# Optimization experiments

Measured on AMD Instinct MI355X. Metric: run time of the kernel, lower is better.

Reference implementation:

```python
import jax, jax.numpy as jnp
import numpy as np

N_E = 8192
E_DIM = 256
BETA = 0.25


def setup_inputs() -> dict:
    key = jax.random.key(0)
    kz, ke = jax.random.split(key)
    z = jax.random.normal(kz, (16, E_DIM, 32, 32), dtype=jnp.float32)
    embedding = jax.random.uniform(ke, (N_E, E_DIM), dtype=jnp.float32,
                                   minval=-1.0 / N_E, maxval=1.0 / N_E)
    return {"z": z, "embedding": embedding}


def reference(z, embedding):
    n_e, e_dim = embedding.shape
    # (B, C, H, W) -> (B, H, W, C) -> (N, e_dim)
    zp = jnp.transpose(z, (0, 2, 3, 1))
    zf = zp.reshape(-1, e_dim)
    # squared L2 distances: |z|^2 + |e|^2 - 2 z.e   -> (N, n_e)
    dists = (jnp.sum(zf * zf, axis=1, keepdims=True)
             + jnp.sum(embedding * embedding, axis=1)
             - 2.0 * (zf @ embedding.T))
    # two smallest distances (top-2 of negated dists)
    _, top2_idx = jax.lax.top_k(-dists, 2)
    min_encoding_indices = top2_idx[:, 0:1]
    second_encoding_indices = top2_idx[:, 1:2]
    min_encodings = jax.nn.one_hot(top2_idx[:, 0], n_e, dtype=zp.dtype)  # (N, n_e)
    z_q = (min_encodings @ embedding).reshape(zp.shape)
    # commitment / codebook loss
    loss = (jnp.mean((jax.lax.stop_gradient(z_q) - zp) ** 2)
            + BETA * jnp.mean((z_q - jax.lax.stop_gradient(zp)) ** 2))
    # straight-through estimator
    z_q = zp + jax.lax.stop_gradient(z_q - zp)
    avg_probs = jnp.mean(min_encodings, axis=0)
    perplexity = jnp.exp(-jnp.sum(avg_probs * jnp.log(avg_probs + 1e-10)))
    z_q = jnp.transpose(z_q, (0, 3, 1, 2))
    return (loss, z_q, perplexity, min_encodings,
            min_encoding_indices, second_encoding_indices)
```

## Files before the change

kernel.cpp:

```cpp
#include <hip/hip_runtime.h>
#include <cfloat>
#include <cstdint>
#include <cstddef>

#define M_ROWS 16384
#define NE     8192
#define KD     256

#define OFF_LOSS   0ULL
#define OFF_ZQ     1ULL
#define OFF_PERP   4194305ULL
#define OFF_ONEHOT 4194306ULL
#define OFF_I0     138412034ULL
#define OFF_I1     138428418ULL

#define SCR_Z16  0ULL
#define SCR_E16  2097152ULL
#define SCR_Z32T 3145728ULL
#define SCR_PART 7340032ULL

#define WS_I0    0
#define WS_HIST  16384
#define WS_ENORM 24576
#define WS_CNORM 32768
#define WS_T0SUM 49152
#define WS_TOTAL 49154

typedef _Float16 fp16x8 __attribute__((ext_vector_type(8)));
typedef float    floatx16 __attribute__((ext_vector_type(16)));

__global__ void zero_ws_kernel(float* __restrict__ ws) {
    int i = blockIdx.x * 256 + threadIdx.x;
    if (i < WS_TOTAL) ws[i] = 0.0f;
}

__global__ void zero_onehot_kernel(float* __restrict__ out) {
    size_t tidg = (size_t)blockIdx.x * 1024 + threadIdx.x;
    float4* base = (float4*)(out + OFF_ONEHOT + 2);
    const float4 zz = make_float4(0.f, 0.f, 0.f, 0.f);
#pragma unroll
    for (int i = 0; i < 8; i++) {
        size_t q = tidg + (size_t)i * 4194304ULL;
        if (q < 33554431ULL) base[q] = zz;
    }
    if (tidg == 0) {
        out[OFF_ONEHOT + 0] = 0.f;
        out[OFF_ONEHOT + 1] = 0.f;
        out[OFF_ONEHOT + 134217726ULL] = 0.f;
        out[OFF_ONEHOT + 134217727ULL] = 0.f;
    }
}

__global__ void scatter_ones_kernel(const int* __restrict__ ws_i0, float* __restrict__ out) {
    int r = blockIdx.x * 256 + threadIdx.x;
    int j = ws_i0[r] & (NE - 1);
    out[OFF_ONEHOT + (size_t)r * NE + j] = 1.0f;
}

__device__ __forceinline__ float pairwise16(const float* sq, int lane16) {
    const int h = lane16 >> 3;
    const int j = lane16 & 7;
    float r = sq[h * 128 + j];
#pragma unroll
    for (int i = 1; i < 16; i++) r = r + sq[h * 128 + i * 8 + j];
    float s = r + __shfl_xor(r, 1);
    s = s + __shfl_xor(s, 2);
    s = s + __shfl_xor(s, 4);
    s = s + __shfl_xor(s, 8);
    return s;
}

__global__ void enorm_kernel(const float* __restrict__ emb, float* __restrict__ enorm) {
    __shared__ float sq[16][257];
    const int tid = threadIdx.x;
    const int row0 = blockIdx.x * 16;
#pragma unroll
    for (int p = 0; p < 4; p++) {
        int q = p * 256 + tid;
        int rl = q >> 6, kq = q & 63;
        float4 v = *(const float4*)(emb + (size_t)(row0 + rl) * KD + kq * 4);
        sq[rl][kq * 4 + 0] = v.x * v.x;
        sq[rl][kq * 4 + 1] = v.y * v.y;
        sq[rl][kq * 4 + 2] = v.z * v.z;
        sq[rl][kq * 4 + 3] = v.w * v.w;
    }
    __syncthreads();
    const int rl = tid >> 4, lane16 = tid & 15;
    float s = pairwise16(&sq[rl][0], lane16);
    if (lane16 == 0) enorm[row0 + rl] = s;
}

__global__ void cnorm_kernel(const float* __restrict__ z, float* __restrict__ cnorm) {
    __shared__ float sq[16][257];
    const int tid = threadIdx.x;
    const int r0  = blockIdx.x * 16;
    const int b   = r0 >> 10;
    const int hw0 = r0 & 1023;
    const float* zb = z + ((size_t)b << 18) + hw0;
#pragma unroll
    for (int p = 0; p < 4; p++) {
        int q = p * 256 + tid;
        int c = q >> 2, hq = q & 3;
        float4 v = *(const float4*)(zb + ((size_t)c << 10) + hq * 4);
        sq[hq * 4 + 0][c] = v.x * v.x;
        sq[hq * 4 + 1][c] = v.y * v.y;
        sq[hq * 4 + 2][c] = v.z * v.z;
        sq[hq * 4 + 3][c] = v.w * v.w;
    }
    __syncthreads();
    const int rl = tid >> 4, lane16 = tid & 15;
    float s = pairwise16(&sq[rl][0], lane16);
    if (lane16 == 0) cnorm[r0 + rl] = s;
}

__global__ void split_z_kernel(const float* __restrict__ z, _Float16* __restrict__ z16,
                               float* __restrict__ z32t) {
    __shared__ float tile[64][65];
    const int tid = threadIdx.x;
    const int r0  = blockIdx.x * 64;
    const int kbig = blockIdx.y;
    const int b   = r0 >> 10;
    const int hw0 = r0 & 1023;
#pragma unroll
    for (int p = 0; p < 4; p++) {
        int q = p * 256 + tid;
        int cl = q >> 4, hq = q & 15;
        float4 v = *(const float4*)(z + ((size_t)b << 18) + (size_t)(kbig * 64 + cl) * 1024 + hw0 + hq * 4);
        tile[hq * 4 + 0][cl] = v.x;
        tile[hq * 4 + 1][cl] = v.y;
        tile[hq * 4 + 2][cl] = v.z;
        tile[hq * 4 + 3][cl] = v.w;
    }
    __syncthreads();
#pragma unroll
    for (int p = 0; p < 2; p++) {
        int u = p * 256 + tid;
        int row = u >> 3, k8l = u & 7;
        int r = r0 + row;
        fp16x8 vh;
#pragma unroll
        for (int e = 0; e < 8; e++) vh[e] = (_Float16)tile[row][k8l * 8 + e];
        int kb = kbig * 2 + (k8l >> 2);
        int k8 = k8l & 3;
        size_t unit = ((size_t)(r >> 7) * 8 + kb) * 512 + (size_t)(r & 127) * 4 + (k8 ^ (r & 3));
        *(fp16x8*)(z16 + unit * 8) = vh;
    }
#pragma unroll
    for (int p = 0; p < 4; p++) {
        int q = p * 256 + tid;
        int row = q >> 4, co = (q & 15) * 4;
        float4 v = make_float4(tile[row][co], tile[row][co + 1], tile[row][co + 2], tile[row][co + 3]);
        *(float4*)(z32t + (size_t)(r0 + row) * 256 + kbig * 64 + co) = v;
    }
}

__global__ void split_e_kernel(const float* __restrict__ emb, _Float16* __restrict__ e16) {
    int u = blockIdx.x * 256 + threadIdx.x;
    size_t go = (size_t)u * 8;
    float4 v0 = *(const float4*)(emb + go);
    float4 v1 = *(const float4*)(emb + go + 4);
    float x[8] = {v0.x, v0.y, v0.z, v0.w, v1.x, v1.y, v1.z, v1.w};
    fp16x8 vh;
#pragma unroll
    for (int e = 0; e < 8; e++) vh[e] = (_Float16)(x[e] * 256.0f);
    int code = u >> 5, k8g = u & 31;
    int kb = k8g >> 2, k8 = k8g & 3;
    size_t unit = ((size_t)(code >> 7) * 8 + kb) * 512 + (size_t)(code & 127) * 4 + (k8 ^ (code & 3));
    *(fp16x8*)(e16 + unit * 8) = vh;
}

__device__ __forceinline__ fp16x8 frag_ld(const _Float16* lds, int rc, int ku) {
    int slot = rc * 4 + (ku ^ (rc & 3));
    return *(const fp16x8*)(lds + slot * 8);
}

#define MFMA(d, a, b) d = __builtin_amdgcn_mfma_f32_32x32x16_f16(a, b, d, 0, 0, 0)

__device__ __forceinline__ void ins2(float t, int i, float& t0, int& i0, float& t1, int& i1) {
    if (t < t0 || (t == t0 && i < i0)) { t1 = t0; i1 = i0; t0 = t; i0 = i; }
    else if (t < t1 || (t == t1 && i < i1)) { t1 = t; i1 = i; }
}

__launch_bounds__(256, 3)
__global__ void mfma_top2_kernel(const _Float16* __restrict__ e16, const _Float16* __restrict__ z16,
                                 const float* __restrict__ enorm_g, const float* __restrict__ cnorm_g,
                                 float4* __restrict__ part) {
    __shared__ _Float16 As[2][4096];
    __shared__ _Float16 Bs[2][4096];
    __shared__ float enb[128];
    __shared__ float mbuf[128][4];

    const int tid = threadIdx.x;
    const int lane = tid & 63, wid = tid >> 6;
    const int l31 = lane & 31, half = lane >> 5;
    const int wave_m = wid & 1, wave_n = wid >> 1;
    const int mtile = blockIdx.x;
    const int ntile = blockIdx.y;

    const float4* Ap = (const float4*)(e16 + (size_t)mtile * 8 * 512 * 8);
    const float4* Bp = (const float4*)(z16 + (size_t)ntile * 8 * 512 * 8);

    if (tid < 128) enb[tid] = enorm_g[mtile * 128 + tid];
    float Cn[2];
    Cn[0] = cnorm_g[ntile * 128 + wave_n * 64 + l31];
    Cn[1] = cnorm_g[ntile * 128 + wave_n * 64 + 32 + l31];

    const int rcA0 = wave_m * 64 + l31, rcA1 = rcA0 + 32;
    const int rcB0 = wave_n * 64 + l31, rcB1 = rcB0 + 32;

    {
        float4 ra0 = Ap[tid], ra1 = Ap[256 + tid];
        float4 rb0 = Bp[tid], rb1 = Bp[256 + tid];
        ((float4*)As[0])[tid] = ra0; ((float4*)As[0])[256 + tid] = ra1;
        ((float4*)Bs[0])[tid] = rb0; ((float4*)Bs[0])[256 + tid] = rb1;
    }
    __syncthreads();

    floatx16 acc00 = (floatx16)0.f, acc01 = (floatx16)0.f,
             acc10 = (floatx16)0.f, acc11 = (floatx16)0.f;

    for (int kb = 0; kb < 8; kb++) {
        const int cur = kb & 1;
        float4 ra0, ra1, rb0, rb1;
        if (kb < 7) {
            const int nb = (kb + 1) * 512;
            ra0 = Ap[nb + tid]; ra1 = Ap[nb + 256 + tid];
            rb0 = Bp[nb + tid]; rb1 = Bp[nb + 256 + tid];
        }
#pragma unroll
        for (int ks = 0; ks < 2; ks++) {
            const int ku = ks * 2 + half;
            fp16x8 a0 = frag_ld(As[cur], rcA0, ku);
            fp16x8 a1 = frag_ld(As[cur], rcA1, ku);
            fp16x8 b0 = frag_ld(Bs[cur], rcB0, ku);
            fp16x8 b1 = frag_ld(Bs[cur], rcB1, ku);
            MFMA(acc00, a0, b0);
            MFMA(acc01, a0, b1);
            MFMA(acc10, a1, b0);
            MFMA(acc11, a1, b1);
        }
        if (kb < 7) {
            ((float4*)As[cur ^ 1])[tid] = ra0; ((float4*)As[cur ^ 1])[256 + tid] = ra1;
            ((float4*)Bs[cur ^ 1])[tid] = rb0; ((float4*)Bs[cur ^ 1])[256 + tid] = rb1;
        }
        __syncthreads();
    }

    float t0s[2] = {FLT_MAX, FLT_MAX}, t1s[2] = {FLT_MAX, FLT_MAX};
    int   i0s[2] = {0x7fffffff, 0x7fffffff}, i1s[2] = {0x7fffffff, 0x7fffffff};
#pragma unroll
    for (int mt = 0; mt < 2; mt++) {
#pragma unroll
        for (int reg = 0; reg < 16; reg++) {
            const int rl = (reg & 3) + 8 * (reg >> 2) + 4 * half;
            const int cloc = wave_m * 64 + mt * 32 + rl;
            const int code = mtile * 128 + cloc;
            const float E = enb[cloc];
            float g0 = (mt == 0) ? acc00[reg] : acc10[reg];
            float g1 = (mt == 0) ? acc01[reg] : acc11[reg];
            ins2(fmaf(-0.0078125f, g0, Cn[0] + E), code, t0s[0], i0s[0], t1s[0], i1s[0]);
            ins2(fmaf(-0.0078125f, g1, Cn[1] + E), code, t0s[1], i0s[1], t1s[1], i1s[1]);
        }
    }
#pragma unroll
    for (int s = 0; s < 2; s++) {
        float o0 = __shfl_xor(t0s[s], 32), o1 = __shfl_xor(t1s[s], 32);
        int  oi0 = __shfl_xor(i0s[s], 32), oi1 = __shfl_xor(i1s[s], 32);
        ins2(o0, oi0, t0s[s], i0s[s], t1s[s], i1s[s]);
        ins2(o1, oi1, t0s[s], i0s[s], t1s[s], i1s[s]);
    }
    __syncthreads();
    if (wave_m == 1 && lane < 32) {
#pragma unroll
        for (int s = 0; s < 2; s++) {
            int zr = wave_n * 64 + s * 32 + l31;
            mbuf[zr][0] = t0s[s]; mbuf[zr][1] = t1s[s];
            mbuf[zr][2] = __int_as_float(i0s[s]); mbuf[zr][3] = __int_as_float(i1s[s]);
        }
    }
    __syncthreads();
    if (wave_m == 0 && lane < 32) {
#pragma unroll
        for (int s = 0; s < 2; s++) {
            int zr = wave_n * 64 + s * 32 + l31;
            ins2(mbuf[zr][0], __float_as_int(mbuf[zr][2]), t0s[s], i0s[s], t1s[s], i1s[s]);
            ins2(mbuf[zr][1], __float_as_int(mbuf[zr][3]), t0s[s], i0s[s], t1s[s], i1s[s]);
            float4 o;
            o.x = t0s[s]; o.y = t1s[s];
            o.z = __int_as_float(i0s[s]); o.w = __int_as_float(i1s[s]);
            part[(size_t)(ntile * 128 + zr) * 64 + mtile] = o;
        }
    }
}

__global__ void rescore_kernel(const float* __restrict__ z32t, const float* __restrict__ emb,
                               const float* __restrict__ enorm_g, const float* __restrict__ cnorm_g,
                               const float4* __restrict__ part, float* __restrict__ out,
                               int* __restrict__ ws_i0, int* __restrict__ hist,
                               double* __restrict__ t0sum) {
    const int tid  = threadIdx.x;
    const int lane = tid & 63, wid = tid >> 6;
    const int r = blockIdx.x * 4 + wid;

    const int c4 = lane * 4;
    float4 zv = *(const float4*)(z32t + (size_t)r * 256 + c4);
    const double zv0 = (double)zv.x, zv1 = (double)zv.y, zv2 = (double)zv.z, zv3 = (double)zv.w;

    float m1 = FLT_MAX, m2 = FLT_MAX;
    for (int g = 0; g < 64; g++) {
        float4 p = part[(size_t)r * 64 + g];
        if (p.x < m1) { m2 = m1; m1 = p.x; } else if (p.x < m2) m2 = p.x;
        if (p.y < m1) { m2 = m1; m1 = p.y; } else if (p.y < m2) m2 = p.y;
    }
    const float T = m2 + 1.2e-4f;
    const float C = cnorm_g[r];

    float bt0 = FLT_MAX, bt1 = FLT_MAX;
    int   bi0 = NE - 1, bi1 = NE - 1;
    for (int g = 0; g < 64; g++) {
        float4 p = part[(size_t)r * 64 + g];
        float tv[2] = {p.x, p.y};
        int   jv[2] = {__float_as_int(p.z), __float_as_int(p.w)};
#pragma unroll
        for (int e = 0; e < 2; e++) {
            if (tv[e] <= T) {
                const int j = jv[e] & (NE - 1);
                float4 ev = *(const float4*)(emb + ((size_t)j << 8) + c4);
                double gl = zv0 * (double)ev.x + zv1 * (double)ev.y +
                            zv2 * (double)ev.z + zv3 * (double)ev.w;
#pragma unroll
                for (int m = 1; m < 64; m <<= 1) gl += __shfl_xor(gl, m);
                float g2 = (float)(2.0 * gl);
                float S = C + enorm_g[j];
                float tex = S - g2;
                if (tex < bt0 || (tex == bt0 && j < bi0)) {
                    bt1 = bt0; bi1 = bi0; bt0 = tex; bi0 = j;
                } else if (tex < bt1 || (tex == bt1 && j < bi1)) {
                    bt1 = tex; bi1 = j;
                }
            }
        }
    }

    if (lane == 0) {
        out[OFF_I0 + r] = (float)bi0;
        out[OFF_I1 + r] = (float)bi1;
        ws_i0[r] = bi0;
        atomicAdd(&hist[bi0], 1);
    }
    __shared__ double red[4];
    if (lane == 0) red[wid] = (double)bt0;
    __syncthreads();
    if (tid == 0) atomicAdd(t0sum, (red[0] + red[1]) + (red[2] + red[3]));
}

__global__ void zq_kernel(const float* __restrict__ emb, const int* __restrict__ ws_i0,
                          float* __restrict__ out) {
    __shared__ float zt[64][65];
    const int tid = threadIdx.x;
    const int r0  = blockIdx.x * 64;
    const int b   = r0 >> 10;
    const int hw0 = r0 & 1023;
    const int kb  = blockIdx.y;
#pragma unroll
    for (int p = 0; p < 4; p++) {
        int q = p * 256 + tid;
        int row = q >> 4, co = (q & 15) * 4;
        int idx = ws_i0[r0 + row] & (NE - 1);
        float4 v = *(const float4*)(emb + ((size_t)idx << 8) + kb * 64 + co);
        zt[row][co + 0] = v.x; zt[row][co + 1] = v.y;
        zt[row][co + 2] = v.z; zt[row][co + 3] = v.w;
    }
    __syncthreads();
#pragma unroll
    for (int p = 0; p < 4; p++) {
        int q = p * 256 + tid;
        int c = q >> 4, h4 = (q & 15) * 4;
        float4 v = make_float4(zt[h4 + 0][c], zt[h4 + 1][c], zt[h4 + 2][c], zt[h4 + 3][c]);
        *(float4*)(out + OFF_ZQ + (((size_t)b * 256 + kb * 64 + c) << 10) + hw0 + h4) = v;
    }
}

__global__ void finalize_kernel(const int* __restrict__ hist, const double* __restrict__ t0sum,
                                float* __restrict__ out) {
    __shared__ float red[256];
    float s = 0.f;
    for (int j = threadIdx.x; j < NE; j += 256) {
        float p = (float)hist[j] * (1.0f / 16384.0f);
        s += p * logf(p + 1e-10f);
    }
    red[threadIdx.x] = s;
    __syncthreads();
    for (int m = 128; m; m >>= 1) {
        if (threadIdx.x < m) red[threadIdx.x] += red[threadIdx.x + m];
        __syncthreads();
    }
    if (threadIdx.x == 0) {
        out[OFF_PERP] = expf(-red[0]);
        out[OFF_LOSS] = 1.25f * (float)(t0sum[0] * (1.0 / 4194304.0));
    }
}

extern "C" void kernel_launch(void* const* d_in, const int* in_sizes, int n_in,
                              void* d_out, int out_size, void* d_ws, size_t ws_size,
                              hipStream_t stream) {
    const float* z   = (const float*)d_in[0];
    const float* emb = (const float*)d_in[1];
    float* out = (float*)d_out;
    float* ws  = (float*)d_ws;

    int*    ws_i0    = (int*)ws + WS_I0;
    int*    ws_hist  = (int*)ws + WS_HIST;
    float*  ws_enorm = ws + WS_ENORM;
    float*  ws_cnorm = ws + WS_CNORM;
    double* ws_t0sum = (double*)(ws + WS_T0SUM);

    float* scr = out + OFF_ONEHOT + 2;
    _Float16* z16 = (_Float16*)(scr + SCR_Z16);
    _Float16* e16 = (_Float16*)(scr + SCR_E16);
    float*  z32t  = scr + SCR_Z32T;
    float4* part  = (float4*)(scr + SCR_PART);

    hipLaunchKernelGGL(zero_ws_kernel, dim3(194), dim3(256), 0, stream, ws);
    hipLaunchKernelGGL(enorm_kernel, dim3(512), dim3(256), 0, stream, emb, ws_enorm);
    hipLaunchKernelGGL(cnorm_kernel, dim3(1024), dim3(256), 0, stream, z, ws_cnorm);
    hipLaunchKernelGGL(split_z_kernel, dim3(256, 4), dim3(256), 0, stream, z, z16, z32t);
    hipLaunchKernelGGL(split_e_kernel, dim3(1024), dim3(256), 0, stream, emb, e16);
    hipLaunchKernelGGL(mfma_top2_kernel, dim3(64, 128), dim3(256), 0, stream,
                       e16, z16, ws_enorm, ws_cnorm, part);
    hipLaunchKernelGGL(rescore_kernel, dim3(4096), dim3(256), 0, stream,
                       z32t, emb, ws_enorm, ws_cnorm, part, out, ws_i0, ws_hist, ws_t0sum);
    hipLaunchKernelGGL(zero_onehot_kernel, dim3(4096), dim3(1024), 0, stream, out);
    hipLaunchKernelGGL(scatter_ones_kernel, dim3(64), dim3(256), 0, stream, ws_i0, out);
    hipLaunchKernelGGL(zq_kernel, dim3(256, 4), dim3(256), 0, stream, emb, ws_i0, out);
    hipLaunchKernelGGL(finalize_kernel, dim3(1), dim3(256), 0, stream,
                       ws_hist, ws_t0sum, out);
}
```

Baseline: 1.160 ms.

## Fuse norm and split kernels, remap GEMM blocks per XCD, parallelize rescore scan

Folds the embedding and z norm kernels and the workspace zeroing into the fp16 split kernels, so each input is read once and fewer kernels are launched. The MFMA top-2 kernel moves to a 1-D grid whose blocks are remapped so that each XCD works on a contiguous group of z tiles, aiming at better L2 reuse, and its occupancy hint is raised from 3 to 4 blocks. The rescore kernel now loads the 64 partial results in parallel across lanes, finds the threshold with a wave-wide shuffle reduction, and visits candidates through ballot masks instead of two serial 64-step loops. The higher occupancy target may force register spills, and the fused split_z kernel uses a large shared-memory tile of about 67 KB per block.

Measured after the change: 1.074 ms. 7.4% less time.

```diff
diff --git a/kernel.cpp b/kernel.cpp
--- a/kernel.cpp
+++ b/kernel.cpp
@@ -29,11 +29,6 @@
 typedef _Float16 fp16x8 __attribute__((ext_vector_type(8)));
 typedef float    floatx16 __attribute__((ext_vector_type(16)));
 
-__global__ void zero_ws_kernel(float* __restrict__ ws) {
-    int i = blockIdx.x * 256 + threadIdx.x;
-    if (i < WS_TOTAL) ws[i] = 0.0f;
-}
-
 __global__ void zero_onehot_kernel(float* __restrict__ out) {
     size_t tidg = (size_t)blockIdx.x * 1024 + threadIdx.x;
     float4* base = (float4*)(out + OFF_ONEHOT + 2);
@@ -57,21 +52,27 @@
     out[OFF_ONEHOT + (size_t)r * NE + j] = 1.0f;
 }
 
-__device__ __forceinline__ float pairwise16(const float* sq, int lane16) {
-    const int h = lane16 >> 3;
-    const int j = lane16 & 7;
-    float r = sq[h * 128 + j];
-#pragma unroll
-    for (int i = 1; i < 16; i++) r = r + sq[h * 128 + i * 8 + j];
-    float s = r + __shfl_xor(r, 1);
-    s = s + __shfl_xor(s, 2);
-    s = s + __shfl_xor(s, 4);
-    s = s + __shfl_xor(s, 8);
+__device__ __forceinline__ float pairwise16_sq(const float* row, int lane16) {
+    const int h = lane16 >> 3, j = lane16 & 7;
+    const float* p = row + h * 128 + j;
+    float x = p[0];
+    float r = __fmul_rn(x, x);
+#pragma unroll
+    for (int i = 1; i < 16; i++) {
+        float y = p[i * 8];
+        r = __fadd_rn(r, __fmul_rn(y, y));
+    }
+    float s = __fadd_rn(r, __shfl_xor(r, 1));
+    s = __fadd_rn(s, __shfl_xor(s, 2));
+    s = __fadd_rn(s, __shfl_xor(s, 4));
+    s = __fadd_rn(s, __shfl_xor(s, 8));
     return s;
 }
 
-__global__ void enorm_kernel(const float* __restrict__ emb, float* __restrict__ enorm) {
-    __shared__ float sq[16][257];
+__global__ void split_e_kernel(const float* __restrict__ emb, _Float16* __restrict__ e16,
+                               float* __restrict__ enorm, int* __restrict__ hist,
+                               float* __restrict__ wsf) {
+    __shared__ float ef[16][261];
     const int tid = threadIdx.x;
     const int row0 = blockIdx.x * 16;
 #pragma unroll
@@ -79,94 +80,73 @@
         int q = p * 256 + tid;
         int rl = q >> 6, kq = q & 63;
         float4 v = *(const float4*)(emb + (size_t)(row0 + rl) * KD + kq * 4);
-        sq[rl][kq * 4 + 0] = v.x * v.x;
-        sq[rl][kq * 4 + 1] = v.y * v.y;
-        sq[rl][kq * 4 + 2] = v.z * v.z;
-        sq[rl][kq * 4 + 3] = v.w * v.w;
-    }
-    __syncthreads();
-    const int rl = tid >> 4, lane16 = tid & 15;
-    float s = pairwise16(&sq[rl][0], lane16);
-    if (lane16 == 0) enorm[row0 + rl] = s;
-}
-
-__global__ void cnorm_kernel(const float* __restrict__ z, float* __restrict__ cnorm) {
-    __shared__ float sq[16][257];
+        ef[rl][kq * 4 + 0] = v.x; ef[rl][kq * 4 + 1] = v.y;
+        ef[rl][kq * 4 + 2] = v.z; ef[rl][kq * 4 + 3] = v.w;
+    }
+    __syncthreads();
+#pragma unroll
+    for (int p = 0; p < 2; p++) {
+        int u = p * 256 + tid;
+        int rl = u >> 5, k8g = u & 31;
+        int code = row0 + rl;
+        fp16x8 vh;
+#pragma unroll
+        for (int e = 0; e < 8; e++) vh[e] = (_Float16)(ef[rl][k8g * 8 + e] * 256.0f);
+        int kb = k8g >> 2, k8 = k8g & 3;
+        size_t unit = ((size_t)(code >> 7) * 8 + kb) * 512 + (size_t)(code & 127) * 4 + (k8 ^ (code & 3));
+        *(fp16x8*)(e16 + unit * 8) = vh;
+    }
+    {
+        int rl = tid >> 4, lane16 = tid & 15;
+        float s = pairwise16_sq(&ef[rl][0], lane16);
+        if (lane16 == 0) enorm[row0 + rl] = s;
+    }
+    if (blockIdx.x < 32) hist[blockIdx.x * 256 + tid] = 0;
+    if (blockIdx.x == 32 && tid < 2) wsf[WS_T0SUM + tid] = 0.0f;
+}
+
+__global__ void split_z_kernel(const float* __restrict__ z, _Float16* __restrict__ z16,
+                               float* __restrict__ z32t, float* __restrict__ cnorm) {
+    __shared__ float zf[64][261];
     const int tid = threadIdx.x;
-    const int r0  = blockIdx.x * 16;
+    const int r0  = blockIdx.x * 64;
     const int b   = r0 >> 10;
     const int hw0 = r0 & 1023;
     const float* zb = z + ((size_t)b << 18) + hw0;
 #pragma unroll
-    for (int p = 0; p < 4; p++) {
+    for (int p = 0; p < 16; p++) {
         int q = p * 256 + tid;
-        int c = q >> 2, hq = q & 3;
+        int c = q >> 4, hq = q & 15;
         float4 v = *(const float4*)(zb + ((size_t)c << 10) + hq * 4);
-        sq[hq * 4 + 0][c] = v.x * v.x;
-        sq[hq * 4 + 1][c] = v.y * v.y;
-        sq[hq * 4 + 2][c] = v.z * v.z;
-        sq[hq * 4 + 3][c] = v.w * v.w;
-    }
-    __syncthreads();
-    const int rl = tid >> 4, lane16 = tid & 15;
-    float s = pairwise16(&sq[rl][0], lane16);
-    if (lane16 == 0) cnorm[r0 + rl] = s;
-}
-
-__global__ void split_z_kernel(const float* __restrict__ z, _Float16* __restrict__ z16,
-                               float* __restrict__ z32t) {
-    __shared__ float tile[64][65];
-    const int tid = threadIdx.x;
-    const int r0  = blockIdx.x * 64;
-    const int kbig = blockIdx.y;
-    const int b   = r0 >> 10;
-    const int hw0 = r0 & 1023;
-#pragma unroll
-    for (int p = 0; p < 4; p++) {
-        int q = p * 256 + tid;
-        int cl = q >> 4, hq = q & 15;
-        float4 v = *(const float4*)(z + ((size_t)b << 18) + (size_t)(kbig * 64 + cl) * 1024 + hw0 + hq * 4);
-        tile[hq * 4 + 0][cl] = v.x;
-        tile[hq * 4 + 1][cl] = v.y;
-        tile[hq * 4 + 2][cl] = v.z;
-        tile[hq * 4 + 3][cl] = v.w;
-    }
-    __syncthreads();
-#pragma unroll
-    for (int p = 0; p < 2; p++) {
+        zf[hq * 4 + 0][c] = v.x; zf[hq * 4 + 1][c] = v.y;
+        zf[hq * 4 + 2][c] = v.z; zf[hq * 4 + 3][c] = v.w;
+    }
+    __syncthreads();
+#pragma unroll
+    for (int rr = 0; rr < 4; rr++) {
+        int row = rr * 16 + (tid >> 4);
+        float s = pairwise16_sq(&zf[row][0], tid & 15);
+        if ((tid & 15) == 0) cnorm[r0 + row] = s;
+    }
+#pragma unroll
+    for (int p = 0; p < 8; p++) {
         int u = p * 256 + tid;
-        int row = u >> 3, k8l = u & 7;
+        int row = u >> 5, k8g = u & 31;
         int r = r0 + row;
         fp16x8 vh;
 #pragma unroll
-        for (int e = 0; e < 8; e++) vh[e] = (_Float16)tile[row][k8l * 8 + e];
-        int kb = kbig * 2 + (k8l >> 2);
-        int k8 = k8l & 3;
+        for (int e = 0; e < 8; e++) vh[e] = (_Float16)zf[row][k8g * 8 + e];
+        int kb = k8g >> 2, k8 = k8g & 3;
         size_t unit = ((size_t)(r >> 7) * 8 + kb) * 512 + (size_t)(r & 127) * 4 + (k8 ^ (r & 3));
         *(fp16x8*)(z16 + unit * 8) = vh;
     }
 #pragma unroll
-    for (int p = 0; p < 4; p++) {
+    for (int p = 0; p < 16; p++) {
         int q = p * 256 + tid;
-        int row = q >> 4, co = (q & 15) * 4;
-        float4 v = make_float4(tile[row][co], tile[row][co + 1], tile[row][co + 2], tile[row][co + 3]);
-        *(float4*)(z32t + (size_t)(r0 + row) * 256 + kbig * 64 + co) = v;
-    }
-}
-
-__global__ void split_e_kernel(const float* __restrict__ emb, _Float16* __restrict__ e16) {
-    int u = blockIdx.x * 256 + threadIdx.x;
-    size_t go = (size_t)u * 8;
-    float4 v0 = *(const float4*)(emb + go);
-    float4 v1 = *(const float4*)(emb + go + 4);
-    float x[8] = {v0.x, v0.y, v0.z, v0.w, v1.x, v1.y, v1.z, v1.w};
-    fp16x8 vh;
-#pragma unroll
-    for (int e = 0; e < 8; e++) vh[e] = (_Float16)(x[e] * 256.0f);
-    int code = u >> 5, k8g = u & 31;
-    int kb = k8g >> 2, k8 = k8g & 3;
-    size_t unit = ((size_t)(code >> 7) * 8 + kb) * 512 + (size_t)(code & 127) * 4 + (k8 ^ (code & 3));
-    *(fp16x8*)(e16 + unit * 8) = vh;
+        int row = q >> 6, co = (q & 63) * 4;
+        float4 v = make_float4(zf[row][co], zf[row][co + 1], zf[row][co + 2], zf[row][co + 3]);
+        *(float4*)(z32t + (size_t)(r0 + row) * 256 + co) = v;
+    }
 }
 
 __device__ __forceinline__ fp16x8 frag_ld(const _Float16* lds, int rc, int ku) {
@@ -181,7 +161,7 @@
     else if (t < t1 || (t == t1 && i < i1)) { t1 = t; i1 = i; }
 }
 
-__launch_bounds__(256, 3)
+__launch_bounds__(256, 4)
 __global__ void mfma_top2_kernel(const _Float16* __restrict__ e16, const _Float16* __restrict__ z16,
                                  const float* __restrict__ enorm_g, const float* __restrict__ cnorm_g,
                                  float4* __restrict__ part) {
@@ -194,8 +174,10 @@
     const int lane = tid & 63, wid = tid >> 6;
     const int l31 = lane & 31, half = lane >> 5;
     const int wave_m = wid & 1, wave_n = wid >> 1;
-    const int mtile = blockIdx.x;
-    const int ntile = blockIdx.y;
+    const int id = blockIdx.x;
+    const int xcd = id & 7, slot = id >> 3;
+    const int mtile = slot >> 4;
+    const int ntile = (xcd << 4) | (slot & 15);
 
     const float4* Ap = (const float4*)(e16 + (size_t)mtile * 8 * 512 * 8);
     const float4* Bp = (const float4*)(z16 + (size_t)ntile * 8 * 512 * 8);
@@ -302,42 +284,47 @@
     const int lane = tid & 63, wid = tid >> 6;
     const int r = blockIdx.x * 4 + wid;
 
+    float4 p = part[(size_t)r * 64 + lane];
+    const float tv0 = p.x, tv1 = p.y;
+    const int jv0 = __float_as_int(p.z), jv1 = __float_as_int(p.w);
+
+    float a = fminf(tv0, tv1), bmx = fmaxf(tv0, tv1);
+#pragma unroll
+    for (int m = 1; m < 64; m <<= 1) {
+        float oa = __shfl_xor(a, m), ob = __shfl_xor(bmx, m);
+        float na = fminf(a, oa);
+        bmx = fminf(fmaxf(a, oa), fminf(bmx, ob));
+        a = na;
+    }
+    const float T = bmx + 1.2e-4f;
+    const float C = cnorm_g[r];
+
     const int c4 = lane * 4;
     float4 zv = *(const float4*)(z32t + (size_t)r * 256 + c4);
     const double zv0 = (double)zv.x, zv1 = (double)zv.y, zv2 = (double)zv.z, zv3 = (double)zv.w;
 
-    float m1 = FLT_MAX, m2 = FLT_MAX;
-    for (int g = 0; g < 64; g++) {
-        float4 p = part[(size_t)r * 64 + g];
-        if (p.x < m1) { m2 = m1; m1 = p.x; } else if (p.x < m2) m2 = p.x;
-        if (p.y < m1) { m2 = m1; m1 = p.y; } else if (p.y < m2) m2 = p.y;
-    }
-    const float T = m2 + 1.2e-4f;
-    const float C = cnorm_g[r];
-
     float bt0 = FLT_MAX, bt1 = FLT_MAX;
     int   bi0 = NE - 1, bi1 = NE - 1;
-    for (int g = 0; g < 64; g++) {
-        float4 p = part[(size_t)r * 64 + g];
-        float tv[2] = {p.x, p.y};
-        int   jv[2] = {__float_as_int(p.z), __float_as_int(p.w)};
-#pragma unroll
-        for (int e = 0; e < 2; e++) {
-            if (tv[e] <= T) {
-                const int j = jv[e] & (NE - 1);
-                float4 ev = *(const float4*)(emb + ((size_t)j << 8) + c4);
-                double gl = zv0 * (double)ev.x + zv1 * (double)ev.y +
-                            zv2 * (double)ev.z + zv3 * (double)ev.w;
-#pragma unroll
-                for (int m = 1; m < 64; m <<= 1) gl += __shfl_xor(gl, m);
-                float g2 = (float)(2.0 * gl);
-                float S = C + enorm_g[j];
-                float tex = S - g2;
-                if (tex < bt0 || (tex == bt0 && j < bi0)) {
-                    bt1 = bt0; bi1 = bi0; bt0 = tex; bi0 = j;
-                } else if (tex < bt1 || (tex == bt1 && j < bi1)) {
-                    bt1 = tex; bi1 = j;
-                }
+    unsigned long long msk[2];
+    msk[0] = __ballot(tv0 <= T);
+    msk[1] = __ballot(tv1 <= T);
+    for (int pass = 0; pass < 2; pass++) {
+        unsigned long long mm = msk[pass];
+        while (mm) {
+            int g = __builtin_ctzll(mm);
+            mm &= mm - 1;
+            int j = __shfl(pass ? jv1 : jv0, g) & (NE - 1);
+            float4 ev = *(const float4*)(emb + ((size_t)j << 8) + c4);
+            double gl = zv0 * (double)ev.x + zv1 * (double)ev.y +
+                        zv2 * (double)ev.z + zv3 * (double)ev.w;
+#pragma unroll
+            for (int m = 1; m < 64; m <<= 1) gl += __shfl_xor(gl, m);
+            float g2 = (float)(2.0 * gl);
+            float tex = (C + enorm_g[j]) - g2;
+            if (tex < bt0 || (tex == bt0 && j < bi0)) {
+                bt1 = bt0; bi1 = bi0; bt0 = tex; bi0 = j;
+            } else if (tex < bt1 || (tex == bt1 && j < bi1)) {
+                bt1 = tex; bi1 = j;
             }
         }
     }
@@ -421,12 +408,11 @@
     float*  z32t  = scr + SCR_Z32T;
     float4* part  = (float4*)(scr + SCR_PART);
 
-    hipLaunchKernelGGL(zero_ws_kernel, dim3(194), dim3(256), 0, stream, ws);
-    hipLaunchKernelGGL(enorm_kernel, dim3(512), dim3(256), 0, stream, emb, ws_enorm);
-    hipLaunchKernelGGL(cnorm_kernel, dim3(1024), dim3(256), 0, stream, z, ws_cnorm);
-    hipLaunchKernelGGL(split_z_kernel, dim3(256, 4), dim3(256), 0, stream, z, z16, z32t);
-    hipLaunchKernelGGL(split_e_kernel, dim3(1024), dim3(256), 0, stream, emb, e16);
-    hipLaunchKernelGGL(mfma_top2_kernel, dim3(64, 128), dim3(256), 0, stream,
+    hipLaunchKernelGGL(split_e_kernel, dim3(512), dim3(256), 0, stream,
+                       emb, e16, ws_enorm, ws_hist, ws);
+    hipLaunchKernelGGL(split_z_kernel, dim3(256), dim3(256), 0, stream,
+                       z, z16, z32t, ws_cnorm);
+    hipLaunchKernelGGL(mfma_top2_kernel, dim3(8192), dim3(256), 0, stream,
                        e16, z16, ws_enorm, ws_cnorm, part);
     hipLaunchKernelGGL(rescore_kernel, dim3(4096), dim3(256), 0, stream,
                        z32t, emb, ws_enorm, ws_cnorm, part, out, ws_i0, ws_hist, ws_t0sum);
```
